# Kernel optimization log

Hardware: AMD Instinct MI355X
Metric: run time of the kernel (lower is better)

Reference implementation:

```python
import jax, jax.numpy as jnp
import numpy as np

PERIOD = 24
TREND_WINDOW = 24
HALF = TREND_WINDOW // 2          # 12
DROP = (TREND_WINDOW - 1) // 2    # 11 rows dropped off the batch axis (as in original)


def setup_inputs() -> dict:
    key = jax.random.key(0)
    x = jax.random.normal(key, (4096, 2048), dtype=jnp.float32)
    return {"x": x}


def _trend(x):
    # Centered moving average with boundary-clipped (variable-size) windows,
    # vectorized via an exclusive cumulative sum.  x: (B, T)
    B, T = x.shape
    cs = jnp.concatenate([jnp.zeros((B, 1), x.dtype), jnp.cumsum(x, axis=1)], axis=1)  # (B, T+1)
    i = jnp.arange(T)
    start = jnp.clip(i - HALF, 0, T)           # max(0, i - half_window)
    end = jnp.clip(i + HALF + 1, 0, T)         # min(T, i + half_window + 1)
    sums = cs[:, end] - cs[:, start]           # (B, T)
    counts = (end - start).astype(x.dtype)     # (T,)
    return sums / counts


def _seasonal(x):
    # Phase-wise mean: seasonal[b, t] = mean_{t' : t' % PERIOD == t % PERIOD} x[b, t']
    B, T = x.shape
    phase = jnp.arange(T) % PERIOD                                    # (T,)
    sums = jax.ops.segment_sum(x.T, phase, num_segments=PERIOD)      # (P, B)
    counts = jax.ops.segment_sum(jnp.ones((T,), x.dtype), phase, num_segments=PERIOD)  # (P,)
    means = sums / counts[:, None]                                    # (P, B)
    return means[phase].T                                             # (B, T)


def reference(x):
    trend = _trend(x)
    detrended = x - trend                 # additive method
    seasonal = _seasonal(detrended)
    residual = x - trend - seasonal
    out = jnp.stack([trend, seasonal, residual], axis=2)  # (B, T, 3)
    # drop_na: original slices along the batch axis
    return out[DROP:, :, :]
```

## Files before the change

### kernel.cpp

```cpp
#include <hip/hip_runtime.h>

#define TT 2048
#define BB 4096
#define DROP_ROWS 11
#define NOUT (BB - DROP_ROWS)
#define PERIOD 24
#define BLOCK 256
#define HALF 12
#define ROWS 4

__global__ __launch_bounds__(BLOCK) void seasonal_decomp_kernel(
    const float* __restrict__ x, float* __restrict__ out) {
  __shared__ float buf[6144];
  __shared__ float wt0[4], wt1[4];
  __shared__ float pp[PERIOD][8];
  __shared__ float pmean[PERIOD];
  float* const cs = buf;
  float* const sd = buf + 2080;
  float* const sout = buf;

  const int tid = threadIdx.x;
  const int lane = tid & 63;
  const int wave = tid >> 6;
  const int rbase = blockIdx.x * ROWS;

  float4 v0, v1;
  if (rbase < NOUT) {
    const float4* rx = (const float4*)(x + (size_t)(rbase + DROP_ROWS) * TT);
    v0 = rx[tid];
    v1 = rx[tid + 256];
  }

  for (int r = 0; r < ROWS; ++r) {
    const int orow_i = rbase + r;
    const bool active = (orow_i < NOUT);

    float s0 = 0.f, s1 = 0.f, i0 = 0.f, i1 = 0.f;
    float tr[8], sdr[8];

    if (active) {
      s0 = v0.x + v0.y + v0.z + v0.w;
      s1 = v1.x + v1.y + v1.z + v1.w;
      i0 = s0; i1 = s1;
      #pragma unroll
      for (int off = 1; off < 64; off <<= 1) {
        float t0 = __shfl_up(i0, off, 64);
        float t1 = __shfl_up(i1, off, 64);
        if (lane >= off) { i0 += t0; i1 += t1; }
      }
      if (lane == 63) { wt0[wave] = i0; wt1[wave] = i1; }
    }
    __syncthreads();

    if (active) {
      float W0 = 0.f, W1 = 0.f, H = 0.f;
      #pragma unroll
      for (int w = 0; w < 4; ++w) {
        float a = wt0[w], b = wt1[w];
        H += a;
        if (w < wave) { W0 += a; W1 += b; }
      }
      const float P0 = W0 + (i0 - s0);
      const float P1 = H + W1 + (i1 - s1);
      float4 c0, c1;
      c0.x = P0; c0.y = P0 + v0.x; c0.z = c0.y + v0.y; c0.w = c0.z + v0.z;
      c1.x = P1; c1.y = P1 + v1.x; c1.z = c1.y + v1.y; c1.w = c1.z + v1.z;
      ((float4*)cs)[tid] = c0;
      ((float4*)cs)[tid + 256] = c1;
      if (tid == 255) cs[TT] = P1 + s1;
    }

    if (r + 1 < ROWS && rbase + r + 1 < NOUT) {
      const float4* rx =
          (const float4*)(x + (size_t)(rbase + r + 1 + DROP_ROWS) * TT);
      v0 = rx[tid];
      v1 = rx[tid + 256];
    }
    __syncthreads();

    if (active) {
      #pragma unroll
      for (int j = 0; j < 8; ++j) {
        const int t = tid + 256 * j;
        const float* p = &cs[t];
        const float xt = p[1] - p[0];
        float trv;
        if (t >= HALF && t < TT - HALF - 1) {
          const float* q = &cs[t - HALF];
          trv = (q[2 * HALF + 1] - q[0]) * (1.0f / 25.0f);
        } else {
          const int a = (t - HALF < 0) ? 0 : t - HALF;
          const int e = (t + HALF + 1 > TT) ? TT : t + HALF + 1;
          trv = (cs[e] - cs[a]) / (float)(e - a);
        }
        tr[j] = trv;
        sdr[j] = xt - trv;
        sd[t] = sdr[j];
      }
    }
    __syncthreads();

    if (active && tid < PERIOD * 8) {
      const int p = tid >> 3, jj = tid & 7;
      const int cnt = (p < 8) ? 86 : 85;
      float s = 0.f;
      for (int m = jj; m < cnt; m += 8) s += sd[p + PERIOD * m];
      pp[p][jj] = s;
    }
    __syncthreads();

    if (active && tid < PERIOD) {
      float s = 0.f;
      #pragma unroll
      for (int j2 = 0; j2 < 8; ++j2) s += pp[tid][j2];
      pmean[tid] = s * ((tid < 8) ? (1.0f / 86.f) : (1.0f / 85.f));
    }
    __syncthreads();

    if (active) {
      int ph = tid % PERIOD;
      #pragma unroll
      for (int j = 0; j < 8; ++j) {
        const int t = tid + 256 * j;
        const float pm = pmean[ph];
        ph += 16; if (ph >= PERIOD) ph -= PERIOD;
        sout[3 * t]     = tr[j];
        sout[3 * t + 1] = pm;
        sout[3 * t + 2] = sdr[j] - pm;
      }
    }
    __syncthreads();

    if (active) {
      float4* orow = (float4*)(out + (size_t)orow_i * (TT * 3));
      const float4* so4 = (const float4*)sout;
      #pragma unroll
      for (int j = 0; j < 6; ++j) orow[tid + 256 * j] = so4[tid + 256 * j];
    }
  }
}

extern "C" void kernel_launch(void* const* d_in, const int* in_sizes, int n_in,
                              void* d_out, int out_size, void* d_ws, size_t ws_size,
                              hipStream_t stream) {
  const float* x = (const float*)d_in[0];
  float* out = (float*)d_out;
  const int grid = (NOUT + ROWS - 1) / ROWS;
  seasonal_decomp_kernel<<<grid, BLOCK, 0, stream>>>(x, out);
}
```

Baseline: 27.58 us.

## Give each wave a contiguous time chunk, reduce phase sums in registers, drop barriers

Time indices are remapped so each wave owns a contiguous 512-sample span. Each thread's eight samples then fall into three fixed phase classes, so it can accumulate detrended partial sums in registers. This removes the shared-memory detrended array, the strided 86-element per-phase loop and one block barrier. The interleaved output is now staged and stored per wave, with no barrier between staging and the global store. The cost is a 32-term serial reduction for each phase mean, plus reliance on per-wave ordering of shared-memory accesses, in a kernel that is likely dominated by output bandwidth.

```diff
diff --git a/kernel.cpp b/kernel.cpp
--- a/kernel.cpp
+++ b/kernel.cpp
@@ -12,17 +12,22 @@
 __global__ __launch_bounds__(BLOCK) void seasonal_decomp_kernel(
     const float* __restrict__ x, float* __restrict__ out) {
   __shared__ float buf[6144];
+  __shared__ float pp2[3][264];
   __shared__ float wt0[4], wt1[4];
-  __shared__ float pp[PERIOD][8];
   __shared__ float pmean[PERIOD];
   float* const cs = buf;
-  float* const sd = buf + 2080;
   float* const sout = buf;
 
   const int tid = threadIdx.x;
   const int lane = tid & 63;
   const int wave = tid >> 6;
   const int rbase = blockIdx.x * ROWS;
+
+  const int q0 = (512 * wave + lane) % 24;
+  int mA, mB, mC;
+  if (q0 < 8)       { mA = 0; mB = 2; mC = 1; }
+  else if (q0 < 16) { mA = 1; mB = 0; mC = 2; }
+  else              { mA = 2; mB = 1; mC = 0; }
 
   float4 v0, v1;
   if (rbase < NOUT) {
@@ -36,8 +41,6 @@
     const bool active = (orow_i < NOUT);
 
     float s0 = 0.f, s1 = 0.f, i0 = 0.f, i1 = 0.f;
-    float tr[8], sdr[8];
-
     if (active) {
       s0 = v0.x + v0.y + v0.z + v0.w;
       s1 = v1.x + v1.y + v1.z + v1.w;
@@ -78,16 +81,16 @@
     }
     __syncthreads();
 
+    float tr[8], sdr[8];
     if (active) {
+      float A = 0.f, B = 0.f, C2 = 0.f;
       #pragma unroll
       for (int j = 0; j < 8; ++j) {
-        const int t = tid + 256 * j;
-        const float* p = &cs[t];
-        const float xt = p[1] - p[0];
+        const int t = 512 * wave + 64 * j + lane;
+        const float xt = cs[t + 1] - cs[t];
         float trv;
         if (t >= HALF && t < TT - HALF - 1) {
-          const float* q = &cs[t - HALF];
-          trv = (q[2 * HALF + 1] - q[0]) * (1.0f / 25.0f);
+          trv = (cs[t + HALF + 1] - cs[t - HALF]) * (1.0f / 25.0f);
         } else {
           const int a = (t - HALF < 0) ? 0 : t - HALF;
           const int e = (t + HALF + 1 > TT) ? TT : t + HALF + 1;
@@ -95,47 +98,42 @@
         }
         tr[j] = trv;
         sdr[j] = xt - trv;
-        sd[t] = sdr[j];
+        if (j % 3 == 0) A += sdr[j];
+        else if (j % 3 == 1) B += sdr[j];
+        else C2 += sdr[j];
       }
-    }
-    __syncthreads();
-
-    if (active && tid < PERIOD * 8) {
-      const int p = tid >> 3, jj = tid & 7;
-      const int cnt = (p < 8) ? 86 : 85;
-      float s = 0.f;
-      for (int m = jj; m < cnt; m += 8) s += sd[p + PERIOD * m];
-      pp[p][jj] = s;
+      pp2[mA][tid] = A;
+      pp2[mB][tid] = B;
+      pp2[mC][tid] = C2;
     }
     __syncthreads();
 
     if (active && tid < PERIOD) {
+      const int c = tid & 7, m = tid >> 3;
       float s = 0.f;
       #pragma unroll
-      for (int j2 = 0; j2 < 8; ++j2) s += pp[tid][j2];
+      for (int k = 0; k < 32; ++k) s += pp2[m][8 * k + c];
       pmean[tid] = s * ((tid < 8) ? (1.0f / 86.f) : (1.0f / 85.f));
     }
     __syncthreads();
 
     if (active) {
-      int ph = tid % PERIOD;
+      float* const mysout = sout + 1536 * wave;
+      int p = q0;
       #pragma unroll
       for (int j = 0; j < 8; ++j) {
-        const int t = tid + 256 * j;
-        const float pm = pmean[ph];
-        ph += 16; if (ph >= PERIOD) ph -= PERIOD;
-        sout[3 * t]     = tr[j];
-        sout[3 * t + 1] = pm;
-        sout[3 * t + 2] = sdr[j] - pm;
+        const int t64 = 64 * j + lane;
+        const float pm = pmean[p];
+        p += 16; if (p >= PERIOD) p -= PERIOD;
+        mysout[3 * t64]     = tr[j];
+        mysout[3 * t64 + 1] = pm;
+        mysout[3 * t64 + 2] = sdr[j] - pm;
       }
-    }
-    __syncthreads();
-
-    if (active) {
+      const float4* so4 = (const float4*)mysout;
       float4* orow = (float4*)(out + (size_t)orow_i * (TT * 3));
-      const float4* so4 = (const float4*)sout;
       #pragma unroll
-      for (int j = 0; j < 6; ++j) orow[tid + 256 * j] = so4[tid + 256 * j];
+      for (int j = 0; j < 6; ++j)
+        orow[384 * wave + 64 * j + lane] = so4[64 * j + lane];
     }
   }
 }
```

After: 26.89 us. 2.5% less time.
